# Kernel optimization log

Measured on AMD Instinct MI355X. Metric: run time of the kernel, lower is better.

The kernel has to match this reference:

```python
import jax, jax.numpy as jnp
import numpy as np

V, E, NH, NL, FF, MAXLEN = 32000, 512, 8, 4, 2048, 80
B, L = 32, 80
EPS = 1e-5


def _ln(x, w, b):
    m = jnp.mean(x, axis=-1, keepdims=True)
    v = jnp.var(x, axis=-1, keepdims=True)
    return (x - m) / jnp.sqrt(v + EPS) * w + b


def _mha(q_in, kv_in, in_w, in_b, out_w, out_b, mask):
    # in_w: [3E, E] packed q/k/v like torch MultiheadAttention
    Bq, Lq, Em = q_in.shape
    Lk = kv_in.shape[1]
    hd = Em // NH
    q = q_in @ in_w[:Em].T + in_b[:Em]
    k = kv_in @ in_w[Em:2 * Em].T + in_b[Em:2 * Em]
    v = kv_in @ in_w[2 * Em:].T + in_b[2 * Em:]
    q = q.reshape(Bq, Lq, NH, hd).transpose(0, 2, 1, 3)
    k = k.reshape(Bq, Lk, NH, hd).transpose(0, 2, 1, 3)
    v = v.reshape(Bq, Lk, NH, hd).transpose(0, 2, 1, 3)
    s = jnp.einsum('bhqd,bhkd->bhqk', q, k) * (1.0 / float(np.sqrt(hd)))
    if mask is not None:
        s = s + mask
    a = jax.nn.softmax(s, axis=-1)
    o = jnp.einsum('bhqk,bhkd->bhqd', a, v).transpose(0, 2, 1, 3).reshape(Bq, Lq, Em)
    return o @ out_w.T + out_b


def _forward(caps, W_in, b_in, pos_emb, sa_in_w, sa_in_b, sa_out_w, sa_out_b,
             ca_in_w, ca_in_b, ca_out_w, ca_out_b, ff1_w, ff1_b, ff2_w, ff2_b,
             ln1_w, ln1_b, ln2_w, ln2_b, ln3_w, ln3_b, out_w, out_b):
    Bc, Lc = caps.shape
    # one-hot encode then dense Linear(vocab -> emb): semantically an embedding gather
    oh = jax.nn.one_hot(caps, V, dtype=jnp.float32)          # [B, L, V]
    x = oh @ W_in.T + b_in + pos_emb[:Lc][None]               # [B, L, E]
    mask = jnp.where(jnp.triu(jnp.ones((Lc, Lc), bool), 1), -jnp.inf, 0.0).astype(jnp.float32)
    mem = jnp.zeros((Bc, 1, E), jnp.float32)
    for i in range(NL):  # post-norm TransformerDecoderLayer (torch default, relu FFN)
        sa = _mha(x, x, sa_in_w[i], sa_in_b[i], sa_out_w[i], sa_out_b[i], mask)
        x = _ln(x + sa, ln1_w[i], ln1_b[i])
        ca = _mha(x, mem, ca_in_w[i], ca_in_b[i], ca_out_w[i], ca_out_b[i], None)
        x = _ln(x + ca, ln2_w[i], ln2_b[i])
        ff = jax.nn.relu(x @ ff1_w[i].T + ff1_b[i]) @ ff2_w[i].T + ff2_b[i]
        x = _ln(x + ff, ln3_w[i], ln3_b[i])
    return x @ out_w.T + out_b                                # [B, L, V]


def setup_inputs() -> dict:
    key = jax.random.key(0)
    ks = jax.random.split(key, 16)
    g = lambda k, shape, s=0.02: jax.random.normal(k, shape, jnp.float32) * s
    caps = jax.random.randint(ks[0], (B, L), 1, V)  # avoid pad_idx=0
    return {
        'caps': caps,
        'W_in': g(ks[1], (E, V)),
        'b_in': jnp.zeros((E,), jnp.float32),
        'pos_emb': g(ks[2], (MAXLEN, E)),
        'sa_in_w': g(ks[3], (NL, 3 * E, E)),
        'sa_in_b': jnp.zeros((NL, 3 * E), jnp.float32),
        'sa_out_w': g(ks[4], (NL, E, E)),
        'sa_out_b': jnp.zeros((NL, E), jnp.float32),
        'ca_in_w': g(ks[5], (NL, 3 * E, E)),
        'ca_in_b': jnp.zeros((NL, 3 * E), jnp.float32),
        'ca_out_w': g(ks[6], (NL, E, E)),
        'ca_out_b': jnp.zeros((NL, E), jnp.float32),
        'ff1_w': g(ks[7], (NL, FF, E)),
        'ff1_b': jnp.zeros((NL, FF), jnp.float32),
        'ff2_w': g(ks[8], (NL, E, FF)),
        'ff2_b': jnp.zeros((NL, E), jnp.float32),
        'ln1_w': jnp.ones((NL, E), jnp.float32),
        'ln1_b': jnp.zeros((NL, E), jnp.float32),
        'ln2_w': jnp.ones((NL, E), jnp.float32),
        'ln2_b': jnp.zeros((NL, E), jnp.float32),
        'ln3_w': jnp.ones((NL, E), jnp.float32),
        'ln3_b': jnp.zeros((NL, E), jnp.float32),
        'out_w': g(ks[9], (V, E)),
        'out_b': jnp.zeros((V,), jnp.float32),
    }


def reference(caps, W_in, b_in, pos_emb, sa_in_w, sa_in_b, sa_out_w, sa_out_b,
              ca_in_w, ca_in_b, ca_out_w, ca_out_b, ff1_w, ff1_b, ff2_w, ff2_b,
              ln1_w, ln1_b, ln2_w, ln2_b, ln3_w, ln3_b, out_w, out_b):
    return _forward(caps, W_in, b_in, pos_emb, sa_in_w, sa_in_b, sa_out_w, sa_out_b,
                    ca_in_w, ca_in_b, ca_out_w, ca_out_b, ff1_w, ff1_b, ff2_w, ff2_b,
                    ln1_w, ln1_b, ln2_w, ln2_b, ln3_w, ln3_b, out_w, out_b)
```

## Files before the change

### kernel.cpp

```cpp
#include <hip/hip_runtime.h>

typedef __attribute__((ext_vector_type(8))) short short8;
typedef __attribute__((ext_vector_type(4))) float floatx4;

__device__ __forceinline__ unsigned short f2bf(float f) {
  union { float f; unsigned int u; } un; un.f = f;
  unsigned int r = un.u + 0x7FFFu + ((un.u >> 16) & 1u);
  return (unsigned short)(r >> 16);
}
__device__ __forceinline__ float bf2f(unsigned short h) {
  union { unsigned int u; float f; } un; un.u = ((unsigned int)h) << 16;
  return un.f;
}

__device__ __forceinline__ void async_ld16(const unsigned short* g, unsigned short* l) {
  __builtin_amdgcn_global_load_lds(
      (const __attribute__((address_space(1))) void*)g,
      (__attribute__((address_space(3))) void*)l, 16, 0, 0);
}

template<int TM, int TN, int OUT_BF16, int RELU>
__global__ __launch_bounds__(256, (TM == 64) ? 3 : 2)
void gemm_bt(const unsigned short* __restrict__ A, const unsigned short* __restrict__ B,
             const float* __restrict__ bias, const float* __restrict__ res,
             void* __restrict__ Cout, int M, int N, int K) {
  constexpr int AELEM = TM * 64;
  constexpr int BELEM = TN * 64;
  constexpr int AIT = AELEM / 2048;
  constexpr int BIT = BELEM / 2048;
  constexpr int LPS = AIT + BIT;
  constexpr int FM = TM / 32;
  constexpr int FN = TN / 32;
  __shared__ __align__(16) unsigned short sA[3][AELEM];
  __shared__ __align__(16) unsigned short sB[3][BELEM];
  const int tid = threadIdx.x;
  const int lane = tid & 63;
  const int wave = tid >> 6;

  const int gx = gridDim.x;
  const int nwg = gx * gridDim.y;
  const int ord = blockIdx.y * gx + blockIdx.x;
  const int qq = nwg >> 3, rr = nwg & 7;
  const int xcd = ord & 7, idx = ord >> 3;
  const int lin = (xcd < rr) ? (xcd * (qq + 1) + idx)
                             : (rr * (qq + 1) + (xcd - rr) * qq + idx);
  const int m0 = (lin % gx) * TM;
  const int n0 = (lin / gx) * TN;

  int a_off[AIT], b_off[BIT], lb[AIT > BIT ? AIT : BIT];
#pragma unroll
  for (int it = 0; it < AIT; it++) {
    int e = it * 2048 + tid * 8;
    int r = e >> 6, cb = (e >> 3) & 7;
    a_off[it] = (m0 + r) * K + ((cb ^ (r & 7)) * 8);
    lb[it] = it * 2048 + wave * 512;
  }
#pragma unroll
  for (int it = 0; it < BIT; it++) {
    int e = it * 2048 + tid * 8;
    int r = e >> 6, cb = (e >> 3) & 7;
    b_off[it] = (n0 + r) * K + ((cb ^ (r & 7)) * 8);
  }

  floatx4 acc[FM][FN];
#pragma unroll
  for (int i = 0; i < FM; i++)
#pragma unroll
    for (int j = 0; j < FN; j++) acc[i][j] = (floatx4){0.f, 0.f, 0.f, 0.f};

  const int nkt = K >> 6;
  const int wm = (wave >> 1) * (TM / 2);
  const int wn = (wave & 1) * (TN / 2);
  const int fr = lane & 15;
  const int q = lane >> 4;

  auto stage = [&](int kt, int buf) {
    const int k0 = kt << 6;
#pragma unroll
    for (int it = 0; it < AIT; it++) async_ld16(A + (size_t)a_off[it] + k0, &sA[buf][lb[it]]);
#pragma unroll
    for (int it = 0; it < BIT; it++) async_ld16(B + (size_t)b_off[it] + k0, &sB[buf][lb[it]]);
  };

  stage(0, 0);
  if (nkt > 1) stage(1, 1);
  if (nkt > 2) stage(2, 2);

  int buf = 0;
  for (int kt = 0; kt < nkt; kt++) {
    const int rem = nkt - 1 - kt;
    if (rem >= 2)      asm volatile("s_waitcnt vmcnt(%0)" :: "n"(2 * LPS) : "memory");
    else if (rem == 1) asm volatile("s_waitcnt vmcnt(%0)" :: "n"(LPS) : "memory");
    else               asm volatile("s_waitcnt vmcnt(0)" ::: "memory");
    __builtin_amdgcn_s_barrier();

    const unsigned short* pA = sA[buf];
    const unsigned short* pB = sB[buf];
#pragma unroll
    for (int kk = 0; kk < 64; kk += 32) {
      short8 af[FM], bfr[FN];
      const int cba = (kk >> 3) + q;
#pragma unroll
      for (int t = 0; t < FM; t++) {
        int ra = wm + t * 16 + fr;
        af[t] = *(const short8*)&pA[ra * 64 + ((cba ^ (ra & 7)) * 8)];
      }
#pragma unroll
      for (int t = 0; t < FN; t++) {
        int rb = wn + t * 16 + fr;
        bfr[t] = *(const short8*)&pB[rb * 64 + ((cba ^ (rb & 7)) * 8)];
      }
#pragma unroll
      for (int i = 0; i < FM; i++)
#pragma unroll
        for (int j = 0; j < FN; j++)
          acc[i][j] = __builtin_amdgcn_mfma_f32_16x16x32_bf16(af[i], bfr[j], acc[i][j], 0, 0, 0);
    }

    asm volatile("s_waitcnt lgkmcnt(0)" ::: "memory");
    __builtin_amdgcn_s_barrier();
    if (kt + 3 < nkt) stage(kt + 3, buf);
    buf = (buf == 2) ? 0 : buf + 1;
  }

#pragma unroll
  for (int i = 0; i < FM; i++) {
#pragma unroll
    for (int j = 0; j < FN; j++) {
#pragma unroll
      for (int rg = 0; rg < 4; rg++) {
        int row = m0 + wm + i * 16 + q * 4 + rg;
        int col = n0 + wn + j * 16 + fr;
        float v = acc[i][j][rg];
        if (bias) v += bias[col];
        if (res)  v += res[(size_t)row * N + col];
        if (RELU) v = v > 0.f ? v : 0.f;
        if (OUT_BF16) ((unsigned short*)Cout)[(size_t)row * N + col] = f2bf(v);
        else          ((float*)Cout)[(size_t)row * N + col] = v;
      }
    }
  }
}

__global__ __launch_bounds__(512)
void embed_kernel(const int* __restrict__ caps, const float* __restrict__ W_in,
                  const float* __restrict__ b_in, const float* __restrict__ pos,
                  float* __restrict__ x, unsigned short* __restrict__ xbf) {
  int pidx = blockIdx.x;
  int l = pidx % 80;
  int tok = caps[pidx];
  int e = threadIdx.x;
  float v = W_in[(size_t)e * 32000 + tok] + b_in[e] + pos[l * 512 + e];
  x[(size_t)pidx * 512 + e] = v;
  xbf[(size_t)pidx * 512 + e] = f2bf(v);
}

__global__ __launch_bounds__(256)
void ln_kernel(const float* __restrict__ in, const float* __restrict__ w,
               const float* __restrict__ b, float* __restrict__ xout,
               unsigned short* __restrict__ xbf) {
  int row = blockIdx.x * 4 + (threadIdx.x >> 6);
  int lane = threadIdx.x & 63;
  const float* p = in + (size_t)row * 512;
  float vals[8];
  float s = 0.f, s2 = 0.f;
#pragma unroll
  for (int j = 0; j < 8; j++) {
    float t = p[lane + j * 64];
    vals[j] = t; s += t; s2 += t * t;
  }
#pragma unroll
  for (int off = 32; off; off >>= 1) { s += __shfl_xor(s, off); s2 += __shfl_xor(s2, off); }
  float mean = s * (1.f / 512.f);
  float inv = rsqrtf(s2 * (1.f / 512.f) - mean * mean + 1e-5f);
#pragma unroll
  for (int j = 0; j < 8; j++) {
    int c = lane + j * 64;
    float y = (vals[j] - mean) * inv * w[c] + b[c];
    xout[(size_t)row * 512 + c] = y;
    xbf[(size_t)row * 512 + c] = f2bf(y);
  }
}

__global__ __launch_bounds__(256)
void ln2x_kernel(const float* __restrict__ in, const float* __restrict__ cav,
                 const float* __restrict__ w1, const float* __restrict__ b1,
                 const float* __restrict__ w2, const float* __restrict__ b2,
                 float* __restrict__ xout, unsigned short* __restrict__ xbf) {
  int row = blockIdx.x * 4 + (threadIdx.x >> 6);
  int lane = threadIdx.x & 63;
  const float* p = in + (size_t)row * 512;
  float vals[8];
  float s = 0.f, s2 = 0.f;
#pragma unroll
  for (int j = 0; j < 8; j++) {
    float t = p[lane + j * 64];
    vals[j] = t; s += t; s2 += t * t;
  }
#pragma unroll
  for (int off = 32; off; off >>= 1) { s += __shfl_xor(s, off); s2 += __shfl_xor(s2, off); }
  float mean = s * (1.f / 512.f);
  float inv = rsqrtf(s2 * (1.f / 512.f) - mean * mean + 1e-5f);
  float s_b = 0.f, s2_b = 0.f;
#pragma unroll
  for (int j = 0; j < 8; j++) {
    int c = lane + j * 64;
    float y = (vals[j] - mean) * inv * w1[c] + b1[c] + cav[c];
    vals[j] = y; s_b += y; s2_b += y * y;
  }
#pragma unroll
  for (int off = 32; off; off >>= 1) { s_b += __shfl_xor(s_b, off); s2_b += __shfl_xor(s2_b, off); }
  float mean2 = s_b * (1.f / 512.f);
  float inv2 = rsqrtf(s2_b * (1.f / 512.f) - mean2 * mean2 + 1e-5f);
#pragma unroll
  for (int j = 0; j < 8; j++) {
    int c = lane + j * 64;
    float y = (vals[j] - mean2) * inv2 * w2[c] + b2[c];
    xout[(size_t)row * 512 + c] = y;
    xbf[(size_t)row * 512 + c] = f2bf(y);
  }
}

__global__ __launch_bounds__(256)
void attn_kernel(const unsigned short* __restrict__ qkv, unsigned short* __restrict__ o) {
  __shared__ __align__(16) unsigned short sq[80][72];
  __shared__ __align__(16) unsigned short sk[80][72];
  __shared__ __align__(16) unsigned short svT[64][96];
  __shared__ __align__(16) unsigned short sp[80][96];
  __shared__ float ss[80][84];
  const int tid = threadIdx.x;
  const int lane = tid & 63;
  const int wave = tid >> 6;
  const int bb = blockIdx.x >> 3, hh = blockIdx.x & 7;
  const unsigned short* base = qkv + (size_t)bb * 80 * 1536 + hh * 64;

  for (int idx = tid; idx < 5120; idx += 256) {
    int r = idx >> 6, c = idx & 63;
    sq[r][c] = base[r * 1536 + c];
    sk[r][c] = base[r * 1536 + 512 + c];
    svT[c][r] = base[r * 1536 + 1024 + c];
  }
  for (int idx = tid; idx < 1024; idx += 256) svT[idx >> 4][80 + (idx & 15)] = 0;
  for (int idx = tid; idx < 1280; idx += 256) sp[idx >> 4][80 + (idx & 15)] = 0;
  __syncthreads();

  const int fr = lane & 15;
  const int q = lane >> 4;

  for (int t = wave; t < 25; t += 4) {
    int i0 = (t / 5) * 16, j0 = (t % 5) * 16;
    floatx4 acc = (floatx4){0.f, 0.f, 0.f, 0.f};
#pragma unroll
    for (int kk = 0; kk < 64; kk += 32) {
      short8 a = *(const short8*)&sq[i0 + fr][kk + q * 8];
      short8 b = *(const short8*)&sk[j0 + fr][kk + q * 8];
      acc = __builtin_amdgcn_mfma_f32_16x16x32_bf16(a, b, acc, 0, 0, 0);
    }
#pragma unroll
    for (int rg = 0; rg < 4; rg++) {
      int row = i0 + q * 4 + rg, col = j0 + fr;
      ss[row][col] = (col <= row) ? acc[rg] * 0.125f : -1e30f;
    }
  }
  __syncthreads();

  if (tid < 80) {
    float mx = -1e30f;
#pragma unroll
    for (int j = 0; j < 80; j++) mx = fmaxf(mx, ss[tid][j]);
    float sum = 0.f;
#pragma unroll
    for (int j = 0; j < 80; j++) { float e = __expf(ss[tid][j] - mx); ss[tid][j] = e; sum += e; }
    float inv = 1.f / sum;
#pragma unroll
    for (int j = 0; j < 80; j++) sp[tid][j] = f2bf(ss[tid][j] * inv);
  }
  __syncthreads();

  for (int t = wave; t < 20; t += 4) {
    int i0 = (t / 4) * 16, d0 = (t % 4) * 16;
    floatx4 acc = (floatx4){0.f, 0.f, 0.f, 0.f};
#pragma unroll
    for (int kk = 0; kk < 96; kk += 32) {
      short8 a = *(const short8*)&sp[i0 + fr][kk + q * 8];
      short8 b = *(const short8*)&svT[d0 + fr][kk + q * 8];
      acc = __builtin_amdgcn_mfma_f32_16x16x32_bf16(a, b, acc, 0, 0, 0);
    }
#pragma unroll
    for (int rg = 0; rg < 4; rg++) {
      int row = i0 + q * 4 + rg;
      o[((size_t)bb * 80 + row) * 512 + hh * 64 + d0 + fr] = f2bf(acc[rg]);
    }
  }
}

__global__ __launch_bounds__(256)
void cavec_kernel(const float* __restrict__ ca_out_w, const float* __restrict__ ca_in_b,
                  const float* __restrict__ ca_out_b, float* __restrict__ cav) {
  int g = blockIdx.x * 4 + (threadIdx.x >> 6);
  int lane = threadIdx.x & 63;
  int l = g >> 9, e = g & 511;
  const float* row = ca_out_w + ((size_t)l * 512 + e) * 512;
  const float* inb = ca_in_b + l * 1536 + 1024;
  float s = 0.f;
#pragma unroll
  for (int j = 0; j < 8; j++) s += row[lane + j * 64] * inb[lane + j * 64];
#pragma unroll
  for (int off = 32; off; off >>= 1) s += __shfl_xor(s, off);
  if (lane == 0) cav[g] = s + ca_out_b[l * 512 + e];
}

__global__ __launch_bounds__(256)
void convert_f2bf(const float* __restrict__ in, unsigned short* __restrict__ out, int n4) {
  int i = blockIdx.x * 256 + threadIdx.x;
  if (i < n4) {
    float4 v = ((const float4*)in)[i];
    ushort4 r;
    r.x = f2bf(v.x); r.y = f2bf(v.y); r.z = f2bf(v.z); r.w = f2bf(v.w);
    ((ushort4*)out)[i] = r;
  }
}

extern "C" void kernel_launch(void* const* d_in, const int* in_sizes, int n_in,
                              void* d_out, int out_size, void* d_ws, size_t ws_size,
                              hipStream_t stream) {
  const int*   caps     = (const int*)d_in[0];
  const float* W_in     = (const float*)d_in[1];
  const float* b_in     = (const float*)d_in[2];
  const float* pos_emb  = (const float*)d_in[3];
  const float* sa_in_w  = (const float*)d_in[4];
  const float* sa_in_b  = (const float*)d_in[5];
  const float* sa_out_w = (const float*)d_in[6];
  const float* sa_out_b = (const float*)d_in[7];
  const float* ca_in_b  = (const float*)d_in[9];
  const float* ca_out_w = (const float*)d_in[10];
  const float* ca_out_b = (const float*)d_in[11];
  const float* ff1_w    = (const float*)d_in[12];
  const float* ff1_b    = (const float*)d_in[13];
  const float* ff2_w    = (const float*)d_in[14];
  const float* ff2_b    = (const float*)d_in[15];
  const float* ln1_w    = (const float*)d_in[16];
  const float* ln1_b    = (const float*)d_in[17];
  const float* ln2_w    = (const float*)d_in[18];
  const float* ln2_b    = (const float*)d_in[19];
  const float* ln3_w    = (const float*)d_in[20];
  const float* ln3_b    = (const float*)d_in[21];
  const float* out_w    = (const float*)d_in[22];
  const float* out_b    = (const float*)d_in[23];

  char* ws = (char*)d_ws;
  size_t off = 0;
  auto alloc = [&](size_t bytes) {
    void* p = ws + off;
    off += (bytes + 255) & ~(size_t)255;
    return p;
  };
  unsigned short* w_sa_in  = (unsigned short*)alloc((size_t)4 * 1536 * 512 * 2);
  unsigned short* w_sa_out = (unsigned short*)alloc((size_t)4 * 512 * 512 * 2);
  unsigned short* w_ff1    = (unsigned short*)alloc((size_t)4 * 2048 * 512 * 2);
  unsigned short* w_ff2    = (unsigned short*)alloc((size_t)4 * 512 * 2048 * 2);
  unsigned short* w_out    = (unsigned short*)alloc((size_t)32000 * 512 * 2);
  float*          x        = (float*)alloc((size_t)2560 * 512 * 4);
  unsigned short* xbf      = (unsigned short*)alloc((size_t)2560 * 512 * 2);
  float*          t        = (float*)alloc((size_t)2560 * 512 * 4);
  unsigned short* qkv      = (unsigned short*)alloc((size_t)2560 * 1536 * 2);
  unsigned short* obf      = (unsigned short*)alloc((size_t)2560 * 512 * 2);
  unsigned short* hbf      = (unsigned short*)alloc((size_t)2560 * 2048 * 2);
  float*          cav      = (float*)alloc((size_t)2048 * 4);

  convert_f2bf<<<(786432 + 255) / 256, 256, 0, stream>>>(sa_in_w, w_sa_in, 786432);
  convert_f2bf<<<(262144 + 255) / 256, 256, 0, stream>>>(sa_out_w, w_sa_out, 262144);
  convert_f2bf<<<(1048576 + 255) / 256, 256, 0, stream>>>(ff1_w, w_ff1, 1048576);
  convert_f2bf<<<(1048576 + 255) / 256, 256, 0, stream>>>(ff2_w, w_ff2, 1048576);
  convert_f2bf<<<(4096000 + 255) / 256, 256, 0, stream>>>(out_w, w_out, 4096000);

  embed_kernel<<<2560, 512, 0, stream>>>(caps, W_in, b_in, pos_emb, x, xbf);
  cavec_kernel<<<512, 256, 0, stream>>>(ca_out_w, ca_in_b, ca_out_b, cav);

  for (int i = 0; i < 4; i++) {
    gemm_bt<128, 64, 1, 0><<<dim3(20, 24), 256, 0, stream>>>(
        xbf, w_sa_in + (size_t)i * 1536 * 512, sa_in_b + i * 1536, nullptr,
        qkv, 2560, 1536, 512);
    attn_kernel<<<256, 256, 0, stream>>>(qkv, obf);
    gemm_bt<64, 64, 0, 0><<<dim3(40, 8), 256, 0, stream>>>(
        obf, w_sa_out + (size_t)i * 512 * 512, sa_out_b + i * 512, x,
        t, 2560, 512, 512);
    ln2x_kernel<<<640, 256, 0, stream>>>(t, cav + i * 512,
        ln1_w + i * 512, ln1_b + i * 512, ln2_w + i * 512, ln2_b + i * 512, x, xbf);
    gemm_bt<128, 64, 1, 1><<<dim3(20, 32), 256, 0, stream>>>(
        xbf, w_ff1 + (size_t)i * 2048 * 512, ff1_b + i * 2048, nullptr,
        hbf, 2560, 2048, 512);
    gemm_bt<64, 64, 0, 0><<<dim3(40, 8), 256, 0, stream>>>(
        hbf, w_ff2 + (size_t)i * 512 * 2048, ff2_b + i * 512, x,
        t, 2560, 512, 2048);
    ln_kernel<<<640, 256, 0, stream>>>(t, ln3_w + i * 512, ln3_b + i * 512, x, xbf);
  }

  gemm_bt<128, 64, 0, 0><<<dim3(20, 500), 256, 0, stream>>>(
      xbf, w_out, out_b, nullptr, (float*)d_out, 2560, 32000, 512);
}
```

Before: 1.154 ms.

## Add weight-stationary vocab projection kernel keeping full 128-row weight slab in LDS

Replaces the final vocab GEMM with a dedicated kernel where each of 250 blocks loads a 128x512 slice of the output weight into LDS once (128 KB) and then streams all 2560 activation rows through it in 64-row double-buffered tiles. This avoids re-reading the large output weight matrix per M tile and cuts per-block setup, but leaves only 250 blocks of 512 threads at one block per CU with small 32x32 per-wave tiles. That lowers parallelism and MFMA work per LDS load, and the stores are scattered fp32 writes.

```diff
diff --git a/kernel.cpp b/kernel.cpp
--- a/kernel.cpp
+++ b/kernel.cpp
@@ -17,6 +17,82 @@
   __builtin_amdgcn_global_load_lds(
       (const __attribute__((address_space(1))) void*)g,
       (__attribute__((address_space(3))) void*)l, 16, 0, 0);
+}
+
+__global__ __launch_bounds__(512, 1)
+void gemm_vocab(const unsigned short* __restrict__ A, const unsigned short* __restrict__ B,
+                const float* __restrict__ bias, float* __restrict__ C, int M, int N) {
+  __shared__ __align__(16) unsigned short sB[65536];
+  __shared__ __align__(16) unsigned short sA[2][4096];
+  const int tid = threadIdx.x;
+  const int lane = tid & 63;
+  const int wave = tid >> 6;
+  const int n0 = blockIdx.x * 128;
+  const int fr = lane & 15;
+  const int q = lane >> 4;
+  const int wm = (wave >> 2) * 32;
+  const int wn = (wave & 3) * 32;
+
+  for (int ro = 0; ro < 16; ro++) {
+    int rr = ro * 8 + wave;
+    async_ld16(B + (size_t)(n0 + rr) * 512 + ((lane ^ (rr & 7)) << 3),
+               &sB[ro * 4096 + wave * 512]);
+  }
+
+  auto stage_a = [&](int s, int buf) {
+    int mt = s >> 3, kt = s & 7;
+    int r = tid >> 3, cb = tid & 7;
+    async_ld16(A + (size_t)(mt * 64 + r) * 512 + (kt << 6) + ((cb ^ (r & 7)) << 3),
+               &sA[buf][wave * 512]);
+  };
+
+  floatx4 acc[2][2];
+#pragma unroll
+  for (int i = 0; i < 2; i++)
+#pragma unroll
+    for (int j = 0; j < 2; j++) acc[i][j] = (floatx4){0.f, 0.f, 0.f, 0.f};
+
+  stage_a(0, 0);
+  const int nsteps = (M >> 6) << 3;
+  for (int s = 0; s < nsteps; s++) {
+    __syncthreads();
+    if (s + 1 < nsteps) stage_a(s + 1, (s + 1) & 1);
+    const unsigned short* pA = sA[s & 1];
+    const int kt = s & 7;
+#pragma unroll
+    for (int kk = 0; kk < 64; kk += 32) {
+      const int cba = (kk >> 3) + q;
+      short8 af[2], bfr[2];
+#pragma unroll
+      for (int t = 0; t < 2; t++) {
+        int ra = wm + t * 16 + fr;
+        af[t] = *(const short8*)&pA[ra * 64 + ((cba ^ (ra & 7)) << 3)];
+        int rb = wn + t * 16 + fr;
+        int cbi = (kt << 3) + cba;
+        bfr[t] = *(const short8*)&sB[rb * 512 + ((cbi ^ (rb & 7)) << 3)];
+      }
+#pragma unroll
+      for (int i = 0; i < 2; i++)
+#pragma unroll
+        for (int j = 0; j < 2; j++)
+          acc[i][j] = __builtin_amdgcn_mfma_f32_16x16x32_bf16(af[i], bfr[j], acc[i][j], 0, 0, 0);
+    }
+    if (kt == 7) {
+      const int mt = s >> 3;
+#pragma unroll
+      for (int i = 0; i < 2; i++)
+#pragma unroll
+        for (int j = 0; j < 2; j++) {
+#pragma unroll
+          for (int rg = 0; rg < 4; rg++) {
+            int row = mt * 64 + wm + i * 16 + q * 4 + rg;
+            int col = n0 + wn + j * 16 + fr;
+            C[(size_t)row * N + col] = acc[i][j][rg] + bias[col];
+          }
+          acc[i][j] = (floatx4){0.f, 0.f, 0.f, 0.f};
+        }
+    }
+  }
 }
 
 template<int TM, int TN, int OUT_BF16, int RELU>
@@ -396,6 +472,5 @@
     ln_kernel<<<640, 256, 0, stream>>>(t, ln3_w + i * 512, ln3_b + i * 512, x, xbf);
   }
 
-  gemm_bt<128, 64, 0, 0><<<dim3(20, 500), 256, 0, stream>>>(
-      xbf, w_out, out_b, nullptr, (float*)d_out, 2560, 32000, 512);
-}
+  gemm_vocab<<<250, 512, 0, stream>>>(xbf, w_out, out_b, (float*)d_out, 2560, 32000);
+}
```

After: 1.122 ms. 1.03x faster.
